# Kernel optimization log

Hardware: AMD Instinct MI355X
Metric: run time of the kernel (lower is better)

## Reference

```python
import jax, jax.numpy as jnp
import numpy as np

B, N, C, H, CLS = 16, 1024, 768, 12, 1000
M = 0.5  # amax init for alpha


def setup_inputs() -> dict:
    key = jax.random.key(0)
    k = jax.random.split(key, 7)
    x = jax.random.normal(k[0], (B, N, C), jnp.float32)
    label = jax.random.randint(k[1], (B,), 0, CLS)
    # alpha is initialized to ones*m in the module; add small noise so gating is non-trivial
    alpha = jnp.ones((CLS, 3 * C), jnp.float32) * M + 0.1 * jax.random.normal(k[2], (CLS, 3 * C), jnp.float32)
    qkv_w = jax.random.normal(k[3], (3 * C, C), jnp.float32) * 0.02
    qkv_b = jax.random.normal(k[4], (3 * C,), jnp.float32) * 0.02
    proj_w = jax.random.normal(k[5], (C, C), jnp.float32) * 0.02
    proj_b = jax.random.normal(k[6], (C,), jnp.float32) * 0.02
    return {"x": x, "label": label, "alpha": alpha, "qkv_w": qkv_w,
            "qkv_b": qkv_b, "proj_w": proj_w, "proj_b": proj_b}


def reference(x, label, alpha, qkv_w, qkv_b, proj_w, proj_b):
    b, n, c = x.shape
    h = H
    hd = c // h
    scale = hd ** -0.5
    # per-sample sigmoid gate over the 3C output rows of the qkv projection
    sig = jax.nn.sigmoid(alpha[label])  # (B, 3C)
    # F.linear(x_i, W * s_i[:,None], b * s_i) == (x_i @ W.T) * s_i + b * s_i
    qkv = jnp.einsum('bnc,dc->bnd', x, qkv_w) * sig[:, None, :] + (qkv_b * sig)[:, None, :]
    qkv = qkv.reshape(b, n, 3, h, hd).transpose(2, 0, 3, 1, 4)  # (3, B, H, N, hd)
    q, k_, v = qkv[0], qkv[1], qkv[2]
    attn = jax.nn.softmax(jnp.einsum('bhqd,bhkd->bhqk', q, k_) * scale, axis=-1)
    out = jnp.einsum('bhqk,bhkd->bhqd', attn, v)          # (B, H, N, hd)
    out = out.transpose(0, 2, 1, 3).reshape(b, n, c)       # (B, N, C)
    out = out @ proj_w.T + proj_b
    return out
```

## Files before the change

kernel.cpp:

```cpp
#include <hip/hip_runtime.h>

typedef __bf16 bf16;
typedef __attribute__((ext_vector_type(8))) __bf16 bf16x8;
typedef __attribute__((ext_vector_type(4))) float floatx4;
typedef __attribute__((ext_vector_type(8))) short short8;
typedef __attribute__((ext_vector_type(4))) short short4v;
typedef unsigned short u16;

#define B_  16
#define N_  1024
#define C_  768
#define H_  12
#define HD_ 64
#define TC_ 2304
#define QSZ (B_ * H_ * N_ * HD_)

__device__ __forceinline__ u16 f2b(float f) { bf16 h = (bf16)f; return __builtin_bit_cast(u16, h); }

typedef __attribute__((address_space(1))) const unsigned int guint;
typedef __attribute__((address_space(3))) unsigned int luint;
__device__ __forceinline__ void gl16(const u16* g, u16* l) {
    __builtin_amdgcn_global_load_lds((guint*)g, (luint*)l, 16, 0, 0);
}

__global__ __launch_bounds__(256) void cvt_swz(
    const float* __restrict__ x, const float* __restrict__ qw,
    const float* __restrict__ pw, u16* __restrict__ xb,
    u16* __restrict__ qwb, u16* __restrict__ pwb)
{
    const int gid = blockIdx.x * 256 + threadIdx.x;
    const int b   = gid & 7;
    const int rb  = gid >> 3;
    const int row = rb / 12, g = rb - row * 12;
    const float* src; u16* dst; int r;
    if (row < 16384)      { src = x;  dst = xb;  r = row; }
    else if (row < 18688) { src = qw; dst = qwb; r = row - 16384; }
    else                  { src = pw; dst = pwb; r = row - 18688; }
    const float* sp = src + (size_t)r * 768 + g * 64 + b * 8;
    floatx4 a = *(const floatx4*)sp;
    floatx4 c = *(const floatx4*)(sp + 4);
    short8 v;
    v[0] = (short)f2b(a[0]); v[1] = (short)f2b(a[1]);
    v[2] = (short)f2b(a[2]); v[3] = (short)f2b(a[3]);
    v[4] = (short)f2b(c[0]); v[5] = (short)f2b(c[1]);
    v[6] = (short)f2b(c[2]); v[7] = (short)f2b(c[3]);
    *(short8*)(dst + (size_t)r * 768 + g * 64 + (b ^ (r & 7)) * 8) = v;
}

template <int MODE>
__global__ __launch_bounds__(512, 2) void gemm256(
    const u16* __restrict__ A, const u16* __restrict__ W,
    const float* __restrict__ bias, const float* __restrict__ alpha,
    const int* __restrict__ label, void* __restrict__ out, u16* __restrict__ vT)
{
    __shared__ __align__(16) u16 sm[65536];
    const int t  = threadIdx.x;
    const int w  = t >> 6, l = t & 63;
    const int lr = l & 15, lq = l >> 4, sw = lr & 7;
    const int wr = w >> 2, wc = w & 3;
    const int id = blockIdx.x;
    const int xcd = id & 7, jj = id >> 3;
    const int n_t = jj >> 3;
    const int m_t = xcd * 8 + (jj & 7);
    const int m0 = m_t << 8, n0 = n_t << 8;

    floatx4 acc[8][4];
#pragma unroll
    for (int a = 0; a < 8; a++)
#pragma unroll
        for (int b = 0; b < 4; b++) acc[a][b] = (floatx4){0.f, 0.f, 0.f, 0.f};

    const int cx8 = (t & 7) * 8;
    const int r0  = t >> 3;

    auto a_gaddr = [&](int r, int kt) -> const u16* {
        const int m = m0 + r;
        if (MODE == 0) return A + m * 768 + kt * 64 + cx8;
        return A + (size_t)((((m >> 10) * H_ + kt) << 10) + (m & 1023)) * HD_ + cx8;
    };
    auto stage = [&](int kt, int b) {
#pragma unroll
        for (int h = 0; h < 2; h++)
#pragma unroll
            for (int p = 0; p < 2; p++) {
                gl16(a_gaddr(h * 128 + p * 64 + r0, kt),
                     sm + (b * 2 + h) * 8192 + p * 4096 + t * 8);
                gl16(W + (n0 + h * 128 + p * 64 + r0) * 768 + kt * 64 + cx8,
                     sm + 32768 + (b * 2 + h) * 8192 + p * 4096 + t * 8);
            }
    };
    auto tile = [&](int b) {
        bf16x8 bfrg[4][2];
#pragma unroll
        for (int nt = 0; nt < 4; nt++)
#pragma unroll
            for (int kc = 0; kc < 2; kc++)
                bfrg[nt][kc] = *(const bf16x8*)(sm + 32768 + (b * 2 + (wc >> 1)) * 8192 +
                                ((wc & 1) * 64 + nt * 16 + lr) * 64 + 8 * ((kc * 4 + lq) ^ sw));
#pragma unroll
        for (int mh = 0; mh < 2; mh++) {
            bf16x8 afrg[4][2];
#pragma unroll
            for (int mi = 0; mi < 4; mi++)
#pragma unroll
                for (int kc = 0; kc < 2; kc++)
                    afrg[mi][kc] = *(const bf16x8*)(sm + (b * 2 + wr) * 8192 +
                                    ((mh * 4 + mi) * 16 + lr) * 64 + 8 * ((kc * 4 + lq) ^ sw));
            __builtin_amdgcn_s_setprio(1);
#pragma unroll
            for (int mi = 0; mi < 4; mi++)
#pragma unroll
                for (int nt = 0; nt < 4; nt++)
#pragma unroll
                    for (int kc = 0; kc < 2; kc++)
                        acc[mh * 4 + mi][nt] = __builtin_amdgcn_mfma_f32_16x16x32_bf16(
                            afrg[mi][kc], bfrg[nt][kc], acc[mh * 4 + mi][nt], 0, 0, 0);
            __builtin_amdgcn_s_setprio(0);
        }
    };
    auto tile_step = [&](int b, bool last) {
        if (last) asm volatile("s_waitcnt vmcnt(0)" ::: "memory");
        else      asm volatile("s_waitcnt vmcnt(8)" ::: "memory");
        __builtin_amdgcn_sched_barrier(0);
        __builtin_amdgcn_s_barrier();
        __builtin_amdgcn_sched_barrier(0);
        tile(b);
        asm volatile("" ::: "memory");
        __builtin_amdgcn_s_barrier();
        __builtin_amdgcn_sched_barrier(0);
    };

    stage(0, 0);
    stage(1, 1);
#pragma unroll 1
    for (int i = 0; i < 5; ++i) {
        tile_step(0, false); stage(2 * i + 2, 0);
        tile_step(1, false); stage(2 * i + 3, 1);
    }
    tile_step(0, false);
    tile_step(1, true);

    if (MODE == 0) {
        const int bI  = m0 >> 10;
        const int lab = label[bI];
        const int which = (n0 >= 1536) ? 2 : (n0 >= 768 ? 1 : 0);
        const int pos0 = (m0 & 1023) + wr * 128;
        const int h = (n0 + wc * 64 - which * 768) >> 6;
        u16* ws = sm + w * 8192;
        float sg[4], bv[4];
#pragma unroll
        for (int nt = 0; nt < 4; nt++) {
            const int d3 = n0 + wc * 64 + nt * 16 + lr;
            sg[nt] = 1.f / (1.f + __expf(-alpha[lab * TC_ + d3]));
            bv[nt] = bias[d3];
        }
        if (which == 2) {
#pragma unroll
            for (int nt = 0; nt < 4; nt++) {
                const int dd = nt * 16 + lr;
#pragma unroll
                for (int mt = 0; mt < 8; mt++)
#pragma unroll
                    for (int i = 0; i < 4; i++) {
                        const int p = mt * 16 + lq * 4 + i;
                        ws[dd * 128 + (p & 64) + 8 * (((p >> 3) & 7) ^ (dd & 7)) + (p & 7)]
                            = f2b((acc[mt][nt][i] + bv[nt]) * sg[nt]);
                    }
            }
#pragma unroll
            for (int it = 0; it < 16; ++it) {
                const int dd = it * 4 + (l >> 4);
                const int ch = l & 15;
                *(short8*)(vT + ((((size_t)(bI * H_ + h) << 6) + dd) << 10) + pos0 + ch * 8)
                    = *(const short8*)(ws + dd * 128 + ch * 8);
            }
        } else {
#pragma unroll
            for (int mt = 0; mt < 8; mt++)
#pragma unroll
                for (int nt = 0; nt < 4; nt++)
#pragma unroll
                    for (int i = 0; i < 4; i++) {
                        const int p = mt * 16 + lq * 4 + i;
                        const int d = nt * 16 + lr;
                        ws[p * 64 + 8 * ((d >> 3) ^ (p & 7)) + (d & 7)]
                            = f2b((acc[mt][nt][i] + bv[nt]) * sg[nt]);
                    }
            u16* ob = (u16*)out + which * QSZ + ((((bI * H_ + h) << 10) + pos0) << 6);
#pragma unroll
            for (int it = 0; it < 16; ++it) {
                const int p = it * 8 + (l >> 3);
                const int ch = l & 7;
                *(short8*)(ob + p * 64 + ch * 8) = *(const short8*)(ws + p * 64 + ch * 8);
            }
        }
    } else {
        float bv[4];
#pragma unroll
        for (int nt = 0; nt < 4; nt++) bv[nt] = bias[n0 + wc * 64 + nt * 16 + lr];
        float* swf = (float*)sm + w * (16 * 68);
        const int rr = l >> 2, c0 = (l & 3) * 16;
#pragma unroll
        for (int mt = 0; mt < 8; mt++) {
#pragma unroll
            for (int nt = 0; nt < 4; nt++)
#pragma unroll
                for (int i = 0; i < 4; i++)
                    swf[(lq * 4 + i) * 68 + nt * 16 + lr] = acc[mt][nt][i] + bv[nt];
            float* drow = (float*)out + (size_t)(m0 + wr * 128 + mt * 16 + rr) * 768
                          + n0 + wc * 64 + c0;
#pragma unroll
            for (int jf = 0; jf < 4; jf++)
                *(floatx4*)(drow + jf * 4) = *(const floatx4*)(swf + rr * 68 + c0 + jf * 4);
        }
    }
}

__global__ __launch_bounds__(256, 4) void attn_fwd(
    u16* __restrict__ qb, const u16* __restrict__ kb, const u16* __restrict__ vtb)
{
    __shared__ __align__(16) u16 sQP[64 * 64];
    __shared__ __align__(16) u16 sK[2][64 * 64];
    __shared__ __align__(16) u16 sVt[2][64 * 64];

    const int t = threadIdx.x, w = t >> 6, l = t & 63;
    const int lr = l & 15, lq = l >> 4;
    const int id = blockIdx.x;
    const int r8 = id & 7, s = id >> 3;
    const int bh = r8 * 24 + (s >> 4);
    const int q0 = (s & 15) << 6;
    const int sw = lr & 7;

    const u16* kgb = kb + bh * (N_ * HD_);
    const u16* vgb = vtb + bh * (HD_ * N_);
    const int vrow = t >> 3, vcol = (t & 7) * 8;

    auto stage = [&](int kt, int bufi) {
        const u16* gk = kgb + kt * 4096;
        gl16(gk + t * 8,        sK[bufi] + t * 8);
        gl16(gk + 2048 + t * 8, sK[bufi] + 2048 + t * 8);
        const u16* gv = vgb + kt * 64;
        gl16(gv + vrow * N_ + vcol,        sVt[bufi] + t * 8);
        gl16(gv + (vrow + 32) * N_ + vcol, sVt[bufi] + 2048 + t * 8);
    };

    u16* qg = qb + (bh * N_ + q0) * HD_;
    gl16(qg + t * 8,        sQP + t * 8);
    gl16(qg + 2048 + t * 8, sQP + 2048 + t * 8);
    stage(0, 0);
    __syncthreads();

    bf16x8 qf[2];
#pragma unroll
    for (int kc = 0; kc < 2; kc++)
        qf[kc] = *(const bf16x8*)(sQP + (w * 16 + lr) * 64 + 8 * ((kc * 4 + lq) ^ sw));

    float l_run = 0.f;
    floatx4 o_acc[4];
#pragma unroll
    for (int nt = 0; nt < 4; nt++) o_acc[nt] = (floatx4){0.f, 0.f, 0.f, 0.f};

#pragma unroll 2
    for (int kt = 0; kt < 16; ++kt) {
        const int cb = kt & 1;
        if (kt < 15) stage(kt + 1, cb ^ 1);

        floatx4 st[4];
#pragma unroll
        for (int mt = 0; mt < 4; mt++) st[mt] = (floatx4){0.f, 0.f, 0.f, 0.f};
        __builtin_amdgcn_s_setprio(1);
#pragma unroll
        for (int kc = 0; kc < 2; kc++) {
#pragma unroll
            for (int mt = 0; mt < 4; mt++) {
                bf16x8 kf = *(const bf16x8*)(sK[cb] + (mt * 16 + lr) * 64 + 8 * ((kc * 4 + lq) ^ sw));
                st[mt] = __builtin_amdgcn_mfma_f32_16x16x32_bf16(kf, qf[kc], st[mt], 0, 0, 0);
            }
        }
        __builtin_amdgcn_s_setprio(0);

        float rs0 = 0.f, rs1 = 0.f;
        u16 pb[4][4];
#pragma unroll
        for (int mt = 0; mt < 4; mt++) {
#pragma unroll
            for (int i = 0; i < 4; i++) {
                const float p = __builtin_amdgcn_exp2f(
                    fmaf(st[mt][i], 0.18033688011112f, -11.54156032711171f));
                pb[mt][i] = f2b(p);
                if (mt & 1) rs1 += p; else rs0 += p;
            }
        }
        float rs = rs0 + rs1;
        rs += __shfl_xor(rs, 16, 64);
        rs += __shfl_xor(rs, 32, 64);
        l_run += rs;
#pragma unroll
        for (int mt = 0; mt < 4; mt++) {
            short4v pk;
#pragma unroll
            for (int i = 0; i < 4; i++) pk[i] = (short)pb[mt][i];
            *(short4v*)(sQP + (w * 16 + lr) * 64 +
                        8 * ((mt * 2 + (lq >> 1)) ^ sw) + (lq & 1) * 4) = pk;
        }
        __builtin_amdgcn_s_setprio(1);
#pragma unroll
        for (int kc = 0; kc < 2; kc++) {
            bf16x8 pf = *(const bf16x8*)(sQP + (w * 16 + lr) * 64 + 8 * ((kc * 4 + lq) ^ sw));
#pragma unroll
            for (int nt = 0; nt < 4; nt++) {
                bf16x8 vf = *(const bf16x8*)(sVt[cb] + (nt * 16 + lr) * 64 + 8 * ((kc * 4 + lq) ^ sw));
                o_acc[nt] = __builtin_amdgcn_mfma_f32_16x16x32_bf16(pf, vf, o_acc[nt], 0, 0, 0);
            }
        }
        __builtin_amdgcn_s_setprio(0);
        __syncthreads();
    }

    const float linv = 1.f / l_run;
#pragma unroll
    for (int nt = 0; nt < 4; nt++) {
#pragma unroll
        for (int i = 0; i < 4; i++) {
            const float lv = __shfl(linv, lq * 4 + i, 64);
            const int row = w * 16 + lq * 4 + i;
            sQP[row * 64 + 8 * ((nt * 2 + (lr >> 3)) ^ (row & 7)) + (lr & 7)] = f2b(o_acc[nt][i] * lv);
        }
    }
    __syncthreads();
#pragma unroll
    for (int i2 = 0; i2 < 2; i2++) {
        const int idx = i2 * 2048 + t * 8;
        *(short8*)(qg + idx) = *(const short8*)(sQP + idx);
    }
}

extern "C" void kernel_launch(void* const* d_in, const int* in_sizes, int n_in,
                              void* d_out, int out_size, void* d_ws, size_t ws_size,
                              hipStream_t stream)
{
    const float* x      = (const float*)d_in[0];
    const int*   label  = (const int*)d_in[1];
    const float* alpha  = (const float*)d_in[2];
    const float* qkv_w  = (const float*)d_in[3];
    const float* qkv_b  = (const float*)d_in[4];
    const float* proj_w = (const float*)d_in[5];
    const float* proj_b = (const float*)d_in[6];

    u16* xb    = (u16*)d_ws;
    u16* qwb   = xb + (size_t)16384 * 768;
    u16* pwb   = qwb + (size_t)2304 * 768;
    u16* qbuf  = pwb + (size_t)768 * 768;
    u16* kbuf  = qbuf + QSZ;
    u16* vtbuf = kbuf + QSZ;

    cvt_swz<<<7296, 256, 0, stream>>>(x, qkv_w, proj_w, xb, qwb, pwb);
    gemm256<0><<<576, 512, 0, stream>>>(xb, qwb, qkv_b, alpha, label, qbuf, vtbuf);
    attn_fwd<<<3072, 256, 0, stream>>>(qbuf, kbuf, vtbuf);
    gemm256<1><<<192, 512, 0, stream>>>(qbuf, pwb, proj_b, nullptr, nullptr, d_out, nullptr);
}
```

Measured before the change: 308.0 us.

## Interleave per-quarter global-to-LDS staging with MFMA quadrants in GEMM main loop

Restructures the GEMM K-loop from a two-tile prefetch with two barriers per step into a four-phase pipeline. Each tile is split into four MFMA quadrants, and the next K tile's A and B halves are staged through LDS in quarters between them, separated by block barriers. The goal is finer overlap of global loads with MFMA work and smaller register fragment sets. The cost is many more s_barrier calls per tile, a prefetch depth of one tile instead of two, and a wait on the first quarter of the next tile's loads before each tile's compute.

```diff
diff --git a/kernel.cpp b/kernel.cpp
--- a/kernel.cpp
+++ b/kernel.cpp
@@ -22,6 +22,9 @@
 __device__ __forceinline__ void gl16(const u16* g, u16* l) {
     __builtin_amdgcn_global_load_lds((guint*)g, (luint*)l, 16, 0, 0);
 }
+
+#define SBAR __builtin_amdgcn_sched_barrier(0)
+#define HBAR __builtin_amdgcn_s_barrier()
 
 __global__ __launch_bounds__(256) void cvt_swz(
     const float* __restrict__ x, const float* __restrict__ qw,
@@ -78,67 +81,84 @@
         if (MODE == 0) return A + m * 768 + kt * 64 + cx8;
         return A + (size_t)((((m >> 10) * H_ + kt) << 10) + (m & 1023)) * HD_ + cx8;
     };
-    auto stage = [&](int kt, int b) {
-#pragma unroll
-        for (int h = 0; h < 2; h++)
-#pragma unroll
-            for (int p = 0; p < 2; p++) {
+    auto stage_half = [&](int kt, int half, int bb) {
+        const int h = half >> 1;
+        if (half & 1) {
+#pragma unroll
+            for (int p = 0; p < 2; p++)
+                gl16(W + (n0 + h * 128 + p * 64 + r0) * 768 + kt * 64 + cx8,
+                     sm + 32768 + (bb * 2 + h) * 8192 + p * 4096 + t * 8);
+        } else {
+#pragma unroll
+            for (int p = 0; p < 2; p++)
                 gl16(a_gaddr(h * 128 + p * 64 + r0, kt),
-                     sm + (b * 2 + h) * 8192 + p * 4096 + t * 8);
-                gl16(W + (n0 + h * 128 + p * 64 + r0) * 768 + kt * 64 + cx8,
-                     sm + 32768 + (b * 2 + h) * 8192 + p * 4096 + t * 8);
-            }
-    };
-    auto tile = [&](int b) {
-        bf16x8 bfrg[4][2];
-#pragma unroll
-        for (int nt = 0; nt < 4; nt++)
+                     sm + (bb * 2 + h) * 8192 + p * 4096 + t * 8);
+        }
+    };
+    auto rdA = [&](bf16x8 (&a)[4][2], int b, int mh) {
+#pragma unroll
+        for (int mi = 0; mi < 4; mi++)
 #pragma unroll
             for (int kc = 0; kc < 2; kc++)
-                bfrg[nt][kc] = *(const bf16x8*)(sm + 32768 + (b * 2 + (wc >> 1)) * 8192 +
-                                ((wc & 1) * 64 + nt * 16 + lr) * 64 + 8 * ((kc * 4 + lq) ^ sw));
-#pragma unroll
-        for (int mh = 0; mh < 2; mh++) {
-            bf16x8 afrg[4][2];
+                a[mi][kc] = *(const bf16x8*)(sm + (b * 2 + wr) * 8192 +
+                            ((mh * 4 + mi) * 16 + lr) * 64 + 8 * ((kc * 4 + lq) ^ sw));
+    };
+    auto rdB = [&](bf16x8 (&bb)[2][2], int b, int nh) {
+#pragma unroll
+        for (int ni = 0; ni < 2; ni++)
+#pragma unroll
+            for (int kc = 0; kc < 2; kc++)
+                bb[ni][kc] = *(const bf16x8*)(sm + 32768 + (b * 2 + (wc >> 1)) * 8192 +
+                             ((wc & 1) * 64 + (nh * 2 + ni) * 16 + lr) * 64 +
+                             8 * ((kc * 4 + lq) ^ sw));
+    };
+    auto qmf = [&](bf16x8 (&a)[4][2], bf16x8 (&bb)[2][2], int mh, int nh) {
+        __builtin_amdgcn_s_setprio(1);
+#pragma unroll
+        for (int kc = 0; kc < 2; kc++)
 #pragma unroll
             for (int mi = 0; mi < 4; mi++)
 #pragma unroll
-                for (int kc = 0; kc < 2; kc++)
-                    afrg[mi][kc] = *(const bf16x8*)(sm + (b * 2 + wr) * 8192 +
-                                    ((mh * 4 + mi) * 16 + lr) * 64 + 8 * ((kc * 4 + lq) ^ sw));
-            __builtin_amdgcn_s_setprio(1);
-#pragma unroll
-            for (int mi = 0; mi < 4; mi++)
-#pragma unroll
-                for (int nt = 0; nt < 4; nt++)
-#pragma unroll
-                    for (int kc = 0; kc < 2; kc++)
-                        acc[mh * 4 + mi][nt] = __builtin_amdgcn_mfma_f32_16x16x32_bf16(
-                            afrg[mi][kc], bfrg[nt][kc], acc[mh * 4 + mi][nt], 0, 0, 0);
-            __builtin_amdgcn_s_setprio(0);
-        }
-    };
-    auto tile_step = [&](int b, bool last) {
-        if (last) asm volatile("s_waitcnt vmcnt(0)" ::: "memory");
-        else      asm volatile("s_waitcnt vmcnt(8)" ::: "memory");
-        __builtin_amdgcn_sched_barrier(0);
-        __builtin_amdgcn_s_barrier();
-        __builtin_amdgcn_sched_barrier(0);
-        tile(b);
-        asm volatile("" ::: "memory");
-        __builtin_amdgcn_s_barrier();
-        __builtin_amdgcn_sched_barrier(0);
-    };
-
-    stage(0, 0);
-    stage(1, 1);
+                for (int ni = 0; ni < 2; ni++)
+                    acc[mh * 4 + mi][nh * 2 + ni] = __builtin_amdgcn_mfma_f32_16x16x32_bf16(
+                        a[mi][kc], bb[ni][kc], acc[mh * 4 + mi][nh * 2 + ni], 0, 0, 0);
+        __builtin_amdgcn_s_setprio(0);
+    };
+
+    auto tile4 = [&](int kt, int b, bool stg) {
+        bf16x8 a[4][2], b0[2][2], b1[2][2];
+        if (stg) { stage_half(kt + 1, 0, b ^ 1);
+                   asm volatile("s_waitcnt vmcnt(2)" ::: "memory"); }
+        else     { asm volatile("s_waitcnt vmcnt(0)" ::: "memory"); }
+        SBAR; HBAR; SBAR;
+        rdA(a, b, 0); rdB(b0, b, 0);
+        qmf(a, b0, 0, 0);
+        SBAR; HBAR; SBAR;
+        rdB(b1, b, 1);
+        if (stg) stage_half(kt + 1, 1, b ^ 1);
+        SBAR; HBAR; SBAR;
+        qmf(a, b1, 0, 1);
+        SBAR; HBAR; SBAR;
+        rdA(a, b, 1);
+        if (stg) stage_half(kt + 1, 2, b ^ 1);
+        SBAR; HBAR; SBAR;
+        qmf(a, b0, 1, 0);
+        SBAR; HBAR; SBAR;
+        if (stg) stage_half(kt + 1, 3, b ^ 1);
+        SBAR; HBAR; SBAR;
+        qmf(a, b1, 1, 1);
+        SBAR; HBAR; SBAR;
+    };
+
+#pragma unroll
+    for (int h = 0; h < 4; h++) stage_half(0, h, 0);
 #pragma unroll 1
-    for (int i = 0; i < 5; ++i) {
-        tile_step(0, false); stage(2 * i + 2, 0);
-        tile_step(1, false); stage(2 * i + 3, 1);
-    }
-    tile_step(0, false);
-    tile_step(1, true);
+    for (int tt = 0; tt < 5; ++tt) {
+        tile4(2 * tt, 0, true);
+        tile4(2 * tt + 1, 1, true);
+    }
+    tile4(10, 0, true);
+    tile4(11, 1, false);
 
     if (MODE == 0) {
         const int bI  = m0 >> 10;
```

Result: no change. 306.9 us (-0.4%).
